# Kernel tuning notes

Measured on AMD Instinct MI355X. Metric: run time of the kernel, lower is better.

Reference implementation:

```python
import jax, jax.numpy as jnp
import numpy as np

WS = 32      # window_size
P = 4        # patch size inside window
HEADS = 8
DIM_HEAD = 64
INNER = HEADS * DIM_HEAD  # 512
SCALE = DIM_HEAD ** -0.5


def setup_inputs() -> dict:
    key = jax.random.key(0)
    k1, k2, k3 = jax.random.split(key, 3)
    B, C, S = 8, 64, 256
    token_dim = P * P * C  # 1024
    x = jax.random.normal(k1, (B, C, S, S), dtype=jnp.float32)
    w_qkv = jax.random.normal(k2, (token_dim, 3 * INNER), dtype=jnp.float32) * (token_dim ** -0.5)
    w_out = jax.random.normal(k3, (INNER, token_dim), dtype=jnp.float32) * (INNER ** -0.5)
    b_out = jnp.zeros((token_dim,), dtype=jnp.float32)
    return {"x": x, "w_qkv": w_qkv, "w_out": w_out, "b_out": b_out}


def reference(x, w_qkv, w_out, b_out):
    B, C, H, W = x.shape
    H1, W1 = H // WS, W // WS
    # --- divide_regions: b c (h1 h) (w1 w) -> (b h1 w1) c h w ---
    xw = x.reshape(B, C, H1, WS, W1, WS).transpose(0, 2, 4, 1, 3, 5)
    xw = xw.reshape(B * H1 * W1, C, WS, WS)          # [n, C, ws, ws]
    n = xw.shape[0]
    nh = WS // P                                      # patches per side
    # patchify window: n c (nh p1) (nw p2) -> n (nh nw) (p1 p2 c)
    t = xw.reshape(n, C, nh, P, nh, P).transpose(0, 2, 4, 3, 5, 1)
    tokens = t.reshape(n, nh * nh, P * P * C)         # [n, T, D]
    # --- attention ---
    qkv = jnp.einsum('ntd,de->nte', tokens, w_qkv)    # [n, T, 3*inner]
    q, k, v = jnp.split(qkv, 3, axis=-1)
    def heads(a):
        return a.reshape(n, -1, HEADS, DIM_HEAD).transpose(0, 2, 1, 3)  # [n,h,T,dh]
    q, k, v = heads(q), heads(k), heads(v)
    attn = jax.nn.softmax(jnp.einsum('nhqd,nhkd->nhqk', q, k) * SCALE, axis=-1)
    o = jnp.einsum('nhqk,nhkd->nhqd', attn, v)        # [n,h,T,dh]
    o = o.transpose(0, 2, 1, 3).reshape(n, nh * nh, INNER)
    o = jnp.einsum('nte,ed->ntd', o, w_out) + b_out   # [n, T, D]
    # un-patchify: n (nh nw) (p1 p2 c) -> n c (nh p1) (nw p2)
    o = o.reshape(n, nh, nh, P, P, C).transpose(0, 5, 1, 3, 2, 4)
    o = o.reshape(n, C, WS, WS)
    # --- combine_regions: (b h1 w1) c h w -> b c (h1 h) (w1 w) ---
    o = o.reshape(B, H1, W1, C, WS, WS).transpose(0, 3, 1, 4, 2, 5)
    return o.reshape(B, C, H, W)
```

## Files before the change

kernel.cpp:

```cpp
#include <hip/hip_runtime.h>
#include <hip/hip_bf16.h>
#include <stdint.h>

typedef __attribute__((ext_vector_type(8))) short short8;
typedef __attribute__((ext_vector_type(4))) float floatx4;

constexpr int TD    = 1024;
constexpr int E3    = 1536;
constexpr int INNER = 512;
constexpr int NW    = 512;
constexpr int M_    = NW * 64;


constexpr size_t OFF_TOKA = 0;
constexpr size_t OFF_QKV  = (size_t)M_ * TD * 2;
constexpr size_t OFF_WQT  = OFF_QKV + (size_t)M_ * E3 * 2;
constexpr size_t OFF_WOT  = OFF_WQT + (size_t)E3 * TD * 2;
constexpr size_t OFF_BO   = OFF_WOT + (size_t)TD * INNER * 2;
constexpr size_t WS_NEED  = OFF_BO + TD * 4;

__device__ __forceinline__ void gl_lds16(const void* g, void* l) {
  __builtin_amdgcn_global_load_lds(
      (const __attribute__((address_space(1))) void*)g,
      (__attribute__((address_space(3))) void*)l, 16, 0, 0);
}

__global__ __launch_bounds__(256) void k_patchify(const float* __restrict__ x,
                                                  __hip_bfloat16* __restrict__ tokA) {
  __shared__ __hip_bfloat16 tok[8][1032];
  const int bid = blockIdx.x;
  const int n = bid >> 3, i = bid & 7;
  const int b = n >> 6, h1 = (n >> 3) & 7, w1 = n & 7;
  const int tid = threadIdx.x;
  for (int it = 0; it < 8; ++it) {
    int idx = it * 256 + tid;
    int w4 = idx & 7, p1 = (idx >> 3) & 3, c = idx >> 5;
    int h = h1 * 32 + i * 4 + p1;
    const float4 v = *(const float4*)&x[(((b * 64 + c) * 256 + h) * 256 + w1 * 32 + w4 * 4)];
    __hip_bfloat16* dst = &tok[w4][c * 16 + p1 * 4];
    dst[0] = __float2bfloat16(v.x);
    dst[1] = __float2bfloat16(v.y);
    dst[2] = __float2bfloat16(v.z);
    dst[3] = __float2bfloat16(v.w);
  }
  __syncthreads();
  for (int it = 0; it < 4; ++it) {
    int idx = it * 256 + tid;
    int ch = idx & 127, j = idx >> 7;
    uint4 v = *(const uint4*)&tok[j][ch * 8];
    *(uint4*)&tokA[(size_t)(n * 64 + i * 8 + j) * 1024 + ch * 8] = v;
  }
}

__global__ __launch_bounds__(256) void k_perm_wqkv(const float* __restrict__ wqkv,
                                                   __hip_bfloat16* __restrict__ wqT) {
  __shared__ __hip_bfloat16 wt[16][1032];
  const int e0 = blockIdx.x * 16, tid = threadIdx.x;
  for (int it = 0; it < 64; ++it) {
    int idx = it * 256 + tid;
    int e = idx & 15, d = idx >> 4;
    float v = wqkv[d * 1536 + e0 + e];
    int p1 = d >> 8, p2 = (d >> 6) & 3, c = d & 63;
    wt[e][c * 16 + p1 * 4 + p2] = __float2bfloat16(v);
  }
  __syncthreads();
  for (int it = 0; it < 8; ++it) {
    int idx = it * 256 + tid;
    int ch = idx & 127, e = idx >> 7;
    uint4 v = *(const uint4*)&wt[e][ch * 8];
    *(uint4*)&wqT[(size_t)(e0 + e) * 1024 + ch * 8] = v;
  }
}

__global__ __launch_bounds__(256) void k_perm_wout(const float* __restrict__ wout,
                                                   __hip_bfloat16* __restrict__ woT) {
  __shared__ __hip_bfloat16 wt[16][1032];
  const int e0 = blockIdx.x * 16, tid = threadIdx.x;
  for (int it = 0; it < 64; ++it) {
    int idx = it * 256 + tid;
    int d = idx & 1023, e = idx >> 10;
    float v = wout[(e0 + e) * 1024 + d];
    int p1 = d >> 8, p2 = (d >> 6) & 3, c = d & 63;
    wt[e][c * 16 + p1 * 4 + p2] = __float2bfloat16(v);
  }
  __syncthreads();
  for (int it = 0; it < 64; ++it) {
    int idx = it * 256 + tid;
    int e = idx & 15, dp = idx >> 4;
    woT[(size_t)dp * 512 + e0 + e] = wt[e][dp];
  }
}

__global__ __launch_bounds__(256) void k_perm_bias(const float* __restrict__ bout,
                                                   float* __restrict__ boP) {
  int dp = blockIdx.x * 256 + threadIdx.x;
  int c = dp >> 4, p1 = (dp >> 2) & 3, p2 = dp & 3;
  boP[dp] = bout[p1 * 256 + p2 * 64 + c];
}

__global__ __launch_bounds__(256) void k_gemm_qkv(const __hip_bfloat16* __restrict__ A,
                                                  const __hip_bfloat16* __restrict__ Bt,
                                                  __hip_bfloat16* __restrict__ Cmat) {
  constexpr int K = 1024, N = 1536;
  __shared__ __hip_bfloat16 As[128 * 64];
  __shared__ __hip_bfloat16 Bs[128 * 64];
  const int tid = threadIdx.x;
  const int n0 = blockIdx.x * 128, m0 = blockIdx.y * 128;
  const int lane = tid & 63, wid = tid >> 6;
  const int wm = wid & 1, wn = wid >> 1;
  const int l15 = lane & 15, quad = lane >> 4;
  const int sx = l15 & 7;
  floatx4 acc[4][4] = {};
  for (int k0 = 0; k0 < K; k0 += 64) {
    __syncthreads();
    for (int it = 0; it < 4; ++it) {
      int ci = it * 256 + tid;
      int r = ci >> 3, chs = ci & 7;
      int ch = chs ^ (r & 7);
      gl_lds16(&A[(size_t)(m0 + r) * K + k0 + ch * 8], (char*)As + ci * 16);
      gl_lds16(&Bt[(size_t)(n0 + r) * K + k0 + ch * 8], (char*)Bs + ci * 16);
    }
    __syncthreads();
#pragma unroll
    for (int kk = 0; kk < 64; kk += 32) {
      const int pos = (((kk >> 3) + quad) ^ sx) * 8;
      short8 af[4], bf[4];
#pragma unroll
      for (int mt = 0; mt < 4; ++mt)
        af[mt] = *(const short8*)&As[(wm * 64 + mt * 16 + l15) * 64 + pos];
#pragma unroll
      for (int nt = 0; nt < 4; ++nt)
        bf[nt] = *(const short8*)&Bs[(wn * 64 + nt * 16 + l15) * 64 + pos];
#pragma unroll
      for (int mt = 0; mt < 4; ++mt)
#pragma unroll
        for (int nt = 0; nt < 4; ++nt)
          acc[mt][nt] = __builtin_amdgcn_mfma_f32_16x16x32_bf16(af[mt], bf[nt], acc[mt][nt], 0, 0, 0);
    }
  }
#pragma unroll
  for (int mt = 0; mt < 4; ++mt)
#pragma unroll
    for (int nt = 0; nt < 4; ++nt) {
      int col = n0 + wn * 64 + nt * 16 + l15;
#pragma unroll
      for (int r = 0; r < 4; ++r) {
        int row = m0 + wm * 64 + mt * 16 + quad * 4 + r;
        Cmat[(size_t)row * N + col] = __float2bfloat16(acc[mt][nt][r]);
      }
    }
}

__global__ __launch_bounds__(256) void k_attn(const __hip_bfloat16* __restrict__ qkv,
                                              __hip_bfloat16* __restrict__ oattn) {
  __shared__ __hip_bfloat16 Qs[64 * 64];
  __shared__ __hip_bfloat16 Ks[64 * 64];
  __shared__ __hip_bfloat16 Vt[64 * 72];
  __shared__ __hip_bfloat16 Ps[64 * 72];
  const int win = blockIdx.x, head = blockIdx.y;
  const int tid = threadIdx.x, lane = tid & 63, wid = tid >> 6;
  const int l15 = lane & 15, quad = lane >> 4;
  const int sx = l15 & 7;
  const size_t base = (size_t)win * 64 * 1536 + head * 64;
  for (int l = 0; l < 2; ++l) {
    int idx = l * 256 + tid;
    int t = idx >> 3, ch = idx & 7;
    const size_t rowb = base + (size_t)t * 1536 + ch * 8;
    uint4 q = *(const uint4*)&qkv[rowb];
    uint4 k = *(const uint4*)&qkv[rowb + 512];
    uint4 v = *(const uint4*)&qkv[rowb + 1024];
    const int pos = (ch ^ (t & 7)) * 8;
    *(uint4*)&Qs[t * 64 + pos] = q;
    *(uint4*)&Ks[t * 64 + pos] = k;
    *(uint4*)&Ps[t * 64 + pos] = v;
  }
  __syncthreads();
  {
    const int t = tid & 63, w = tid >> 6;
#pragma unroll
    for (int jn = 0; jn < 2; ++jn) {
      int j = w * 2 + jn;
      short8 v = *(const short8*)&Ps[t * 64 + ((j ^ (t & 7)) * 8)];
#pragma unroll
      for (int jj = 0; jj < 8; ++jj) Vt[(j * 8 + jj) * 72 + t] = ((__hip_bfloat16*)&v)[jj];
    }
  }
  __syncthreads();
  floatx4 sacc[4] = {};
#pragma unroll
  for (int kk = 0; kk < 64; kk += 32) {
    const int pos = (((kk >> 3) + quad) ^ sx) * 8;
    short8 aq = *(const short8*)&Qs[(wid * 16 + l15) * 64 + pos];
#pragma unroll
    for (int ct = 0; ct < 4; ++ct) {
      short8 bk = *(const short8*)&Ks[(ct * 16 + l15) * 64 + pos];
      sacc[ct] = __builtin_amdgcn_mfma_f32_16x16x32_bf16(aq, bk, sacc[ct], 0, 0, 0);
    }
  }
#pragma unroll
  for (int ct = 0; ct < 4; ++ct)
#pragma unroll
    for (int r = 0; r < 4; ++r) sacc[ct][r] = sacc[ct][r] * 0.125f;
#pragma unroll
  for (int r = 0; r < 4; ++r) {
    float m = fmaxf(fmaxf(sacc[0][r], sacc[1][r]), fmaxf(sacc[2][r], sacc[3][r]));
    m = fmaxf(m, __shfl_xor(m, 1));
    m = fmaxf(m, __shfl_xor(m, 2));
    m = fmaxf(m, __shfl_xor(m, 4));
    m = fmaxf(m, __shfl_xor(m, 8));
    float ev[4]; float s0 = 0.f;
#pragma unroll
    for (int ct = 0; ct < 4; ++ct) { ev[ct] = __expf(sacc[ct][r] - m); s0 += ev[ct]; }
    s0 += __shfl_xor(s0, 1);
    s0 += __shfl_xor(s0, 2);
    s0 += __shfl_xor(s0, 4);
    s0 += __shfl_xor(s0, 8);
    float inv = 1.0f / s0;
    int row = wid * 16 + quad * 4 + r;
#pragma unroll
    for (int ct = 0; ct < 4; ++ct)
      Ps[row * 72 + ct * 16 + l15] = __float2bfloat16(ev[ct] * inv);
  }
  __syncthreads();
  floatx4 oacc[4] = {};
#pragma unroll
  for (int kk = 0; kk < 64; kk += 32) {
    const int q8 = quad * 8;
    short8 ap = *(const short8*)&Ps[(wid * 16 + l15) * 72 + kk + q8];
#pragma unroll
    for (int nt = 0; nt < 4; ++nt) {
      short8 bv = *(const short8*)&Vt[(nt * 16 + l15) * 72 + kk + q8];
      oacc[nt] = __builtin_amdgcn_mfma_f32_16x16x32_bf16(ap, bv, oacc[nt], 0, 0, 0);
    }
  }
#pragma unroll
  for (int nt = 0; nt < 4; ++nt) {
    int dh = nt * 16 + l15;
#pragma unroll
    for (int r = 0; r < 4; ++r) {
      int t = wid * 16 + quad * 4 + r;
      oattn[((size_t)win * 64 + t) * 512 + head * 64 + dh] = __float2bfloat16(oacc[nt][r]);
    }
  }
}

__global__ __launch_bounds__(256) void k_gemm_out(const __hip_bfloat16* __restrict__ A,
                                                  const __hip_bfloat16* __restrict__ Bt,
                                                  const float* __restrict__ bias,
                                                  float* __restrict__ out) {
  constexpr int K = 512;
  __shared__ __hip_bfloat16 As[128 * 64];
  __shared__ __hip_bfloat16 Bs[128 * 64];
  const int tid = threadIdx.x;
  const int n0 = blockIdx.x * 128, m0 = blockIdx.y * 128;
  const int lane = tid & 63, wid = tid >> 6;
  const int wm = wid & 1, wn = wid >> 1;
  const int l15 = lane & 15, quad = lane >> 4;
  const int sx = l15 & 7;
  floatx4 acc[4][4] = {};
  for (int k0 = 0; k0 < K; k0 += 64) {
    __syncthreads();
    for (int it = 0; it < 4; ++it) {
      int ci = it * 256 + tid;
      int r = ci >> 3, chs = ci & 7;
      int ch = chs ^ (r & 7);
      gl_lds16(&A[(size_t)(m0 + r) * K + k0 + ch * 8], (char*)As + ci * 16);
      gl_lds16(&Bt[(size_t)(n0 + r) * K + k0 + ch * 8], (char*)Bs + ci * 16);
    }
    __syncthreads();
#pragma unroll
    for (int kk = 0; kk < 64; kk += 32) {
      const int pos = (((kk >> 3) + quad) ^ sx) * 8;
      short8 af[4], bf[4];
#pragma unroll
      for (int mt = 0; mt < 4; ++mt)
        af[mt] = *(const short8*)&As[(wm * 64 + mt * 16 + l15) * 64 + pos];
#pragma unroll
      for (int nt = 0; nt < 4; ++nt)
        bf[nt] = *(const short8*)&Bs[(wn * 64 + nt * 16 + l15) * 64 + pos];
#pragma unroll
      for (int mt = 0; mt < 4; ++mt)
#pragma unroll
        for (int nt = 0; nt < 4; ++nt)
          acc[mt][nt] = __builtin_amdgcn_mfma_f32_16x16x32_bf16(af[mt], bf[nt], acc[mt][nt], 0, 0, 0);
    }
  }
#pragma unroll
  for (int nt = 0; nt < 4; ++nt) {
    int dp = n0 + wn * 64 + nt * 16 + l15;
    float bv = bias[dp];
    int c = dp >> 4, p1 = (dp >> 2) & 3, p2 = dp & 3;
#pragma unroll
    for (int mt = 0; mt < 4; ++mt)
#pragma unroll
      for (int r = 0; r < 4; ++r) {
        int m = m0 + wm * 64 + mt * 16 + quad * 4 + r;
        int win = m >> 6, t = m & 63;
        int i = t >> 3, j = t & 7;
        int b = win >> 6, h1 = (win >> 3) & 7, w1 = win & 7;
        int h = h1 * 32 + i * 4 + p1, w = w1 * 32 + j * 4 + p2;
        out[((b * 64 + c) * 256 + h) * 256 + w] = acc[mt][nt][r] + bv;
      }
  }
}

extern "C" void kernel_launch(void* const* d_in, const int* in_sizes, int n_in,
                              void* d_out, int out_size, void* d_ws, size_t ws_size,
                              hipStream_t stream) {
  const float* x    = (const float*)d_in[0];
  const float* wqkv = (const float*)d_in[1];
  const float* wout = (const float*)d_in[2];
  const float* bout = (const float*)d_in[3];
  float* out = (float*)d_out;
  char* ws = (char*)d_ws;
  if (ws_size < WS_NEED) return;

  __hip_bfloat16* tokA  = (__hip_bfloat16*)(ws + OFF_TOKA);
  __hip_bfloat16* oattn = (__hip_bfloat16*)(ws + OFF_TOKA);
  __hip_bfloat16* qkv   = (__hip_bfloat16*)(ws + OFF_QKV);
  __hip_bfloat16* wqT   = (__hip_bfloat16*)(ws + OFF_WQT);
  __hip_bfloat16* woT   = (__hip_bfloat16*)(ws + OFF_WOT);
  float* boP = (float*)(ws + OFF_BO);

  k_perm_wqkv<<<96, 256, 0, stream>>>(wqkv, wqT);
  k_perm_wout<<<32, 256, 0, stream>>>(wout, woT);
  k_perm_bias<<<4, 256, 0, stream>>>(bout, boP);
  k_patchify<<<4096, 256, 0, stream>>>(x, tokA);
  k_gemm_qkv<<<dim3(12, 256), 256, 0, stream>>>(tokA, wqT, qkv);
  k_attn<<<dim3(512, 8), 256, 0, stream>>>(qkv, oattn);
  k_gemm_out<<<dim3(8, 256), 256, 0, stream>>>(oattn, woT, boP, out);
}
```

Measured before the change: 487.2 us.

## Rewrite QKV and output GEMMs as 256x256 double-buffered pipelined tiles

Both projection GEMMs now share a device routine that works on 256x256 tiles with 512 threads and two LDS buffers. Global-to-LDS staging of the next K tile is interleaved across eight compute phases with explicit barriers, waitcnt, sched_barrier and setprio. A block-index swizzle is added to improve L2 reuse. The aim is to hide load latency and raise MFMA utilisation. The cost is 128KB of LDS per block and more accumulator registers, which limits occupancy and makes the hand-tuned sync fragile.

```diff
diff --git a/kernel.cpp b/kernel.cpp
--- a/kernel.cpp
+++ b/kernel.cpp
@@ -98,55 +98,127 @@
   boP[dp] = bout[p1 * 256 + p2 * 64 + c];
 }
 
-__global__ __launch_bounds__(256) void k_gemm_qkv(const __hip_bfloat16* __restrict__ A,
+template<int K>
+__device__ __forceinline__ void gemm256_acc(
+    const __hip_bfloat16* __restrict__ A,
+    const __hip_bfloat16* __restrict__ Bt,
+    int m0, int n0, int tid,
+    __hip_bfloat16 (*As)[256][64], __hip_bfloat16 (*Bs)[256][64],
+    floatx4 (&acc)[8][4])
+{
+  const int lane = tid & 63, wid = tid >> 6;
+  const int wm = wid >> 2, wn = wid & 3;
+  const int l15 = lane & 15, quad = lane >> 4;
+
+  auto stageB = [&](int tile, int half, int buf) {
+#pragma unroll
+    for (int j = 0; j < 2; ++j) {
+      int idx = j * 512 + tid;
+      int rl = idx >> 3, slot = idx & 7;
+      int r = half * 128 + rl;
+      int ch = slot ^ (r & 7);
+      gl_lds16(&Bt[(size_t)(n0 + r) * K + tile * 64 + ch * 8],
+               (char*)&Bs[buf][0][0] + half * 16384 + idx * 16);
+    }
+  };
+  auto stageA = [&](int tile, int chunk, int buf) {
+#pragma unroll
+    for (int j = 0; j < 2; ++j) {
+      int rl = tid >> 3, slot = tid & 7;
+      int r = j * 128 + chunk * 64 + rl;
+      int ch = slot ^ (r & 7);
+      gl_lds16(&A[(size_t)(m0 + r) * K + tile * 64 + ch * 8],
+               (char*)&As[buf][0][0] + j * 16384 + chunk * 8192 + tid * 16);
+    }
+  };
+
+  short8 bf[4][2];
+
+#define PH(BUF, Q, STAGE, VMW)                                                    \
+  do {                                                                            \
+    short8 af[2][2];                                                              \
+    _Pragma("unroll") for (int m2 = 0; m2 < 2; ++m2) {                            \
+      const int r = wm * 128 + (2 * (Q) + m2) * 16 + l15;                         \
+      _Pragma("unroll") for (int kh = 0; kh < 2; ++kh)                            \
+        af[m2][kh] = *(const short8*)&As[BUF][r][((kh * 4 + quad) ^ (r & 7)) * 8];\
+    }                                                                             \
+    if ((Q) == 0) {                                                               \
+      _Pragma("unroll") for (int n = 0; n < 4; ++n) {                             \
+        const int rb = wn * 64 + n * 16 + l15;                                    \
+        _Pragma("unroll") for (int kh = 0; kh < 2; ++kh)                          \
+          bf[n][kh] = *(const short8*)&Bs[BUF][rb][((kh * 4 + quad) ^ (rb & 7)) * 8];\
+      }                                                                           \
+    }                                                                             \
+    STAGE;                                                                        \
+    __builtin_amdgcn_s_barrier();                                                 \
+    asm volatile("s_waitcnt lgkmcnt(0)" ::: "memory");                            \
+    __builtin_amdgcn_sched_barrier(0);                                            \
+    __builtin_amdgcn_s_setprio(1);                                                \
+    _Pragma("unroll") for (int kh = 0; kh < 2; ++kh)                              \
+      _Pragma("unroll") for (int m2 = 0; m2 < 2; ++m2)                            \
+        _Pragma("unroll") for (int n = 0; n < 4; ++n)                             \
+          acc[2 * (Q) + m2][n] = __builtin_amdgcn_mfma_f32_16x16x32_bf16(         \
+              af[m2][kh], bf[n][kh], acc[2 * (Q) + m2][n], 0, 0, 0);              \
+    __builtin_amdgcn_s_setprio(0);                                                \
+    __builtin_amdgcn_sched_barrier(0);                                            \
+    VMW;                                                                          \
+    __builtin_amdgcn_s_barrier();                                                 \
+    __builtin_amdgcn_sched_barrier(0);                                            \
+  } while (0)
+
+  stageB(0, 0, 0); stageB(0, 1, 0); stageA(0, 0, 0); stageA(0, 1, 0);
+  stageB(1, 0, 1); stageB(1, 1, 1); stageA(1, 0, 1);
+  asm volatile("s_waitcnt vmcnt(6)" ::: "memory");
+  __builtin_amdgcn_s_barrier();
+  __builtin_amdgcn_sched_barrier(0);
+
+  constexpr int NIT = K / 128;
+#pragma unroll 1
+  for (int i = 0; i < NIT - 1; ++i) {
+    const int t1 = 2 * i + 1, t2 = 2 * i + 2, t3 = 2 * i + 3;
+    PH(0, 0, stageA(t1, 1, 1), );
+    PH(0, 1, stageB(t2, 0, 0), );
+    PH(0, 2, stageB(t2, 1, 0), );
+    PH(0, 3, stageA(t2, 0, 0), asm volatile("s_waitcnt vmcnt(6)" ::: "memory"));
+    PH(1, 0, stageA(t2, 1, 0), );
+    PH(1, 1, stageB(t3, 0, 1), );
+    PH(1, 2, stageB(t3, 1, 1), );
+    PH(1, 3, stageA(t3, 0, 1), asm volatile("s_waitcnt vmcnt(6)" ::: "memory"));
+  }
+  PH(0, 0, stageA(2 * NIT - 1, 1, 1), );
+  PH(0, 1, , );
+  PH(0, 2, , );
+  PH(0, 3, , asm volatile("s_waitcnt vmcnt(0)" ::: "memory"));
+  PH(1, 0, , );
+  PH(1, 1, , );
+  PH(1, 2, , );
+  PH(1, 3, , );
+#undef PH
+}
+
+__global__ __launch_bounds__(512) void k_gemm_qkv(const __hip_bfloat16* __restrict__ A,
                                                   const __hip_bfloat16* __restrict__ Bt,
                                                   __hip_bfloat16* __restrict__ Cmat) {
-  constexpr int K = 1024, N = 1536;
-  __shared__ __hip_bfloat16 As[128 * 64];
-  __shared__ __hip_bfloat16 Bs[128 * 64];
+  __shared__ __hip_bfloat16 As[2][256][64];
+  __shared__ __hip_bfloat16 Bs[2][256][64];
   const int tid = threadIdx.x;
-  const int n0 = blockIdx.x * 128, m0 = blockIdx.y * 128;
+  const int bid = blockIdx.x;
+  const int swz = (bid & 7) * 96 + (bid >> 3);
+  const int n0 = (swz % 6) * 256, m0 = (swz / 6) * 256;
+  floatx4 acc[8][4] = {};
+  gemm256_acc<1024>(A, Bt, m0, n0, tid, As, Bs, acc);
   const int lane = tid & 63, wid = tid >> 6;
-  const int wm = wid & 1, wn = wid >> 1;
+  const int wm = wid >> 2, wn = wid & 3;
   const int l15 = lane & 15, quad = lane >> 4;
-  const int sx = l15 & 7;
-  floatx4 acc[4][4] = {};
-  for (int k0 = 0; k0 < K; k0 += 64) {
-    __syncthreads();
-    for (int it = 0; it < 4; ++it) {
-      int ci = it * 256 + tid;
-      int r = ci >> 3, chs = ci & 7;
-      int ch = chs ^ (r & 7);
-      gl_lds16(&A[(size_t)(m0 + r) * K + k0 + ch * 8], (char*)As + ci * 16);
-      gl_lds16(&Bt[(size_t)(n0 + r) * K + k0 + ch * 8], (char*)Bs + ci * 16);
-    }
-    __syncthreads();
-#pragma unroll
-    for (int kk = 0; kk < 64; kk += 32) {
-      const int pos = (((kk >> 3) + quad) ^ sx) * 8;
-      short8 af[4], bf[4];
-#pragma unroll
-      for (int mt = 0; mt < 4; ++mt)
-        af[mt] = *(const short8*)&As[(wm * 64 + mt * 16 + l15) * 64 + pos];
-#pragma unroll
-      for (int nt = 0; nt < 4; ++nt)
-        bf[nt] = *(const short8*)&Bs[(wn * 64 + nt * 16 + l15) * 64 + pos];
-#pragma unroll
-      for (int mt = 0; mt < 4; ++mt)
-#pragma unroll
-        for (int nt = 0; nt < 4; ++nt)
-          acc[mt][nt] = __builtin_amdgcn_mfma_f32_16x16x32_bf16(af[mt], bf[nt], acc[mt][nt], 0, 0, 0);
-    }
-  }
-#pragma unroll
-  for (int mt = 0; mt < 4; ++mt)
+#pragma unroll
+  for (int mt = 0; mt < 8; ++mt)
 #pragma unroll
     for (int nt = 0; nt < 4; ++nt) {
-      int col = n0 + wn * 64 + nt * 16 + l15;
+      const int col = n0 + wn * 64 + nt * 16 + l15;
 #pragma unroll
       for (int r = 0; r < 4; ++r) {
-        int row = m0 + wm * 64 + mt * 16 + quad * 4 + r;
-        Cmat[(size_t)row * N + col] = __float2bfloat16(acc[mt][nt][r]);
+        const int row = m0 + wm * 128 + mt * 16 + quad * 4 + r;
+        Cmat[(size_t)row * 1536 + col] = __float2bfloat16(acc[mt][nt][r]);
       }
     }
 }
@@ -244,61 +316,35 @@
   }
 }
 
-__global__ __launch_bounds__(256) void k_gemm_out(const __hip_bfloat16* __restrict__ A,
+__global__ __launch_bounds__(512) void k_gemm_out(const __hip_bfloat16* __restrict__ A,
                                                   const __hip_bfloat16* __restrict__ Bt,
                                                   const float* __restrict__ bias,
                                                   float* __restrict__ out) {
-  constexpr int K = 512;
-  __shared__ __hip_bfloat16 As[128 * 64];
-  __shared__ __hip_bfloat16 Bs[128 * 64];
+  __shared__ __hip_bfloat16 As[2][256][64];
+  __shared__ __hip_bfloat16 Bs[2][256][64];
   const int tid = threadIdx.x;
-  const int n0 = blockIdx.x * 128, m0 = blockIdx.y * 128;
+  const int bid = blockIdx.x;
+  const int swz = (bid & 7) * 64 + (bid >> 3);
+  const int n0 = (swz & 3) * 256, m0 = (swz >> 2) * 256;
+  floatx4 acc[8][4] = {};
+  gemm256_acc<512>(A, Bt, m0, n0, tid, As, Bs, acc);
   const int lane = tid & 63, wid = tid >> 6;
-  const int wm = wid & 1, wn = wid >> 1;
+  const int wm = wid >> 2, wn = wid & 3;
   const int l15 = lane & 15, quad = lane >> 4;
-  const int sx = l15 & 7;
-  floatx4 acc[4][4] = {};
-  for (int k0 = 0; k0 < K; k0 += 64) {
-    __syncthreads();
-    for (int it = 0; it < 4; ++it) {
-      int ci = it * 256 + tid;
-      int r = ci >> 3, chs = ci & 7;
-      int ch = chs ^ (r & 7);
-      gl_lds16(&A[(size_t)(m0 + r) * K + k0 + ch * 8], (char*)As + ci * 16);
-      gl_lds16(&Bt[(size_t)(n0 + r) * K + k0 + ch * 8], (char*)Bs + ci * 16);
-    }
-    __syncthreads();
-#pragma unroll
-    for (int kk = 0; kk < 64; kk += 32) {
-      const int pos = (((kk >> 3) + quad) ^ sx) * 8;
-      short8 af[4], bf[4];
-#pragma unroll
-      for (int mt = 0; mt < 4; ++mt)
-        af[mt] = *(const short8*)&As[(wm * 64 + mt * 16 + l15) * 64 + pos];
-#pragma unroll
-      for (int nt = 0; nt < 4; ++nt)
-        bf[nt] = *(const short8*)&Bs[(wn * 64 + nt * 16 + l15) * 64 + pos];
-#pragma unroll
-      for (int mt = 0; mt < 4; ++mt)
-#pragma unroll
-        for (int nt = 0; nt < 4; ++nt)
-          acc[mt][nt] = __builtin_amdgcn_mfma_f32_16x16x32_bf16(af[mt], bf[nt], acc[mt][nt], 0, 0, 0);
-    }
-  }
 #pragma unroll
   for (int nt = 0; nt < 4; ++nt) {
-    int dp = n0 + wn * 64 + nt * 16 + l15;
-    float bv = bias[dp];
-    int c = dp >> 4, p1 = (dp >> 2) & 3, p2 = dp & 3;
-#pragma unroll
-    for (int mt = 0; mt < 4; ++mt)
+    const int dp = n0 + wn * 64 + nt * 16 + l15;
+    const float bv = bias[dp];
+    const int c = dp >> 4, p1 = (dp >> 2) & 3, p2 = dp & 3;
+#pragma unroll
+    for (int mt = 0; mt < 8; ++mt)
 #pragma unroll
       for (int r = 0; r < 4; ++r) {
-        int m = m0 + wm * 64 + mt * 16 + quad * 4 + r;
-        int win = m >> 6, t = m & 63;
-        int i = t >> 3, j = t & 7;
-        int b = win >> 6, h1 = (win >> 3) & 7, w1 = win & 7;
-        int h = h1 * 32 + i * 4 + p1, w = w1 * 32 + j * 4 + p2;
+        const int m = m0 + wm * 128 + mt * 16 + quad * 4 + r;
+        const int win = m >> 6, t = m & 63;
+        const int i = t >> 3, j = t & 7;
+        const int b = win >> 6, h1 = (win >> 3) & 7, w1 = win & 7;
+        const int h = h1 * 32 + i * 4 + p1, w = w1 * 32 + j * 4 + p2;
         out[((b * 64 + c) * 256 + h) * 256 + w] = acc[mt][nt][r] + bv;
       }
   }
@@ -326,7 +372,7 @@
   k_perm_wout<<<32, 256, 0, stream>>>(wout, woT);
   k_perm_bias<<<4, 256, 0, stream>>>(bout, boP);
   k_patchify<<<4096, 256, 0, stream>>>(x, tokA);
-  k_gemm_qkv<<<dim3(12, 256), 256, 0, stream>>>(tokA, wqT, qkv);
+  k_gemm_qkv<<<768, 512, 0, stream>>>(tokA, wqT, qkv);
   k_attn<<<dim3(512, 8), 256, 0, stream>>>(qkv, oattn);
-  k_gemm_out<<<dim3(8, 256), 256, 0, stream>>>(oattn, woT, boP, out);
-}
+  k_gemm_out<<<512, 512, 0, stream>>>(oattn, woT, boP, out);
+}
```

After: 443.6 us. 1.1x faster.
